# Kernel tuning notes

Hardware: AMD Instinct MI355X
Metric: run time of the kernel (lower is better)

Reference implementation:

```python
import jax, jax.numpy as jnp
import numpy as np

R = 4        # in_transformations == out_transformations
FS = 3       # filter_size
PAD = 1
STRIDE = 1


def setup_inputs() -> dict:
    key = jax.random.key(0)
    k1, k2, k3 = jax.random.split(key, 3)
    B, Cin, O, K = 16, 64, 64, 4
    Ctot = Cin * R  # 256
    x = jax.random.normal(k1, (B, Ctot, 64, 64), dtype=jnp.float32)
    # kernel bank: [num_dynamic_kernels, out_channels, in_channels, f, f]
    kernel_bank = jax.random.normal(k2, (K, O, Cin, FS, FS), dtype=jnp.float32) * 0.05
    # routing fc: Linear(total_in_channels -> num_kernels)
    fc_w = jax.random.normal(k3, (K, Ctot), dtype=jnp.float32) * 0.05
    fc_b = jnp.zeros((K,), dtype=jnp.float32)
    return {"x": x, "kernel_bank": kernel_bank, "fc_w": fc_w, "fc_b": fc_b}


def reference(x, kernel_bank, fc_w, fc_b):
    B, Ctot, H, W = x.shape
    K, O, Cin, f, _ = kernel_bank.shape
    # --- dynamic routing: global avg pool -> fc -> sigmoid ---
    pooled = x.mean(axis=(2, 3))                                  # [B, Ctot]
    coeffs = jax.nn.sigmoid(pooled @ fc_w.T + fc_b)               # [B, K]
    # --- per-sample kernel synthesis ---
    base = jnp.einsum('bk,kocij->bocij', coeffs, kernel_bank)     # [B, O, Cin, f, f]
    # rotations rot90^k for k in 0..R-1 (matches torch.rot90 dims=(-2,-1))
    rotated = jnp.stack([jnp.rot90(base, k, axes=(-2, -1)) for k in range(R)], axis=1)  # [B, R, O, Cin, f, f]
    # block kernel: block (r_out, r_in) uses rotation index (r_out - r_in) % R,
    # so the r_in sum of convs becomes one conv over all R*Cin input channels.
    r_out = jnp.arange(R)[:, None]
    r_in = jnp.arange(R)[None, :]
    idx = (r_out - r_in) % R                                      # [R, R]
    big = rotated[:, idx]                                         # [B, R_out, R_in, O, Cin, f, f]
    big = big.transpose(0, 1, 3, 2, 4, 5, 6).reshape(B, R * O, R * Cin, f, f)
    # --- per-sample conv (vmapped over batch; each sample has its own kernel) ---
    def conv_one(xi, wi):
        return jax.lax.conv_general_dilated(
            xi[None], wi,
            window_strides=(STRIDE, STRIDE),
            padding=[(PAD, PAD), (PAD, PAD)],
            dimension_numbers=('NCHW', 'OIHW', 'NCHW'))[0]
    return jax.vmap(conv_one)(x, big)                             # [B, R*O, H, W]
```

## Files before the change

kernel.cpp:

```cpp
#include <hip/hip_runtime.h>
#include <hip/hip_bf16.h>
#include <math.h>

#define BATCH 16
#define CT    256
#define HW    64
#define OCH   64
#define NK    4
#define HP    66
#define NPIX  4356

typedef __attribute__((ext_vector_type(4)))  float  f32x4;
typedef __attribute__((ext_vector_type(8)))  short  s16x8;
typedef __attribute__((ext_vector_type(4)))  unsigned short u16x4;

#define GLOBAL_AS __attribute__((address_space(1)))
#define LDS_AS    __attribute__((address_space(3)))

__device__ __constant__ int c_rotsrc[4][9] = {
    {0,1,2,3,4,5,6,7,8},
    {2,5,8,1,4,7,0,3,6},
    {8,7,6,5,4,3,2,1,0},
    {6,3,0,7,4,1,8,5,2}
};

static __device__ inline unsigned short f2bf(float f) {
    union { __hip_bfloat16 h; unsigned short u; } cv;
    cv.h = __float2bfloat16(f);
    return cv.u;
}

__global__ __launch_bounds__(256) void xpose_pool(const float* __restrict__ x,
                                                  unsigned short* __restrict__ xTg,
                                                  float* __restrict__ partial) {
    const int ci0 = blockIdx.x * 64;
    const int g0  = ci0 >> 3;
    const int pr  = blockIdx.y;
    const int b   = blockIdx.z;
    const int t   = threadIdx.x;

    if (pr == 0 || pr == HP-1) {
        for (int u = t; u < 8*HP; u += 256) {
            int g = u / HP, c = u % HP;
            *(s16x8*)(xTg + ((((size_t)(b*32 + g0 + g))*NPIX) + pr*HP + c)*8) =
                (s16x8)(short)0;
        }
        return;
    }
    const int r = pr - 1;

    __shared__ unsigned short tile[64][70];
    const int cilH = t >> 4;
    const int c0   = (t & 15) * 4;
    #pragma unroll
    for (int i = 0; i < 4; ++i) {
        int cil = cilH + i*16;
        f32x4 v = *(const f32x4*)(x + (((size_t)(b*CT + ci0 + cil))*HW + r)*HW + c0);
        tile[cil][c0+0] = f2bf(v[0]);
        tile[cil][c0+1] = f2bf(v[1]);
        tile[cil][c0+2] = f2bf(v[2]);
        tile[cil][c0+3] = f2bf(v[3]);
        float s = v[0] + v[1] + v[2] + v[3];
        s += __shfl_xor(s, 1, 16);
        s += __shfl_xor(s, 2, 16);
        s += __shfl_xor(s, 4, 16);
        s += __shfl_xor(s, 8, 16);
        if ((t & 15) == 0)
            partial[((size_t)(b*HW) + r)*CT + ci0 + cil] = s;
    }
    __syncthreads();

    if (t < 16) {
        int g = t & 7, side = t >> 3;
        *(s16x8*)(xTg + ((((size_t)(b*32 + g0 + g))*NPIX) + pr*HP + side*(HP-1))*8) =
            (s16x8)(short)0;
    }
    #pragma unroll
    for (int i = 0; i < 4; ++i) {
        int u = i*256 + t;
        int c = u & 63, cil0 = (u >> 6) * 4;
        u16x4 w;
        w[0] = tile[cil0+0][c];
        w[1] = tile[cil0+1][c];
        w[2] = tile[cil0+2][c];
        w[3] = tile[cil0+3][c];
        *(u16x4*)(xTg + ((((size_t)(b*32 + g0 + (cil0>>3)))*NPIX) + pr*HP + c + 1)*8
                  + (cil0 & 4)) = w;
    }
}

__global__ __launch_bounds__(256) void coeff_kernel(const float* __restrict__ partial,
                                                    const float* __restrict__ fc_w,
                                                    const float* __restrict__ fc_b,
                                                    float* __restrict__ coeffs) {
    const int b = blockIdx.x;
    const int t = threadIdx.x;
    const float* pp = partial + (size_t)b*HW*CT + t;
    float s = 0.f;
    #pragma unroll 8
    for (int r = 0; r < HW; ++r) s += pp[(size_t)r*CT];
    __shared__ float pool[CT];
    pool[t] = s * (1.f / (HW*HW));
    __syncthreads();
    const int w = t >> 6, l = t & 63;
    float d = 0.f;
    for (int c = l; c < CT; c += 64) d += pool[c] * fc_w[w*CT + c];
    for (int off = 32; off; off >>= 1) d += __shfl_down(d, off, 64);
    if (l == 0)
        coeffs[b*NK + w] = 1.f / (1.f + expf(-(d + fc_b[w])));
}

__global__ __launch_bounds__(256) void bankrot_kernel(const float* __restrict__ bank,
                                                      float* __restrict__ P) {
    const int idx = blockIdx.x * 256 + threadIdx.x;
    const int o = idx & 63;
    const int c = (idx >> 6) & 63;
    const int k = idx >> 12;
    const float* bp = bank + ((size_t)((k*OCH + o)*64 + c))*9;
    float v[9];
    #pragma unroll
    for (int s = 0; s < 9; ++s) v[s] = bp[s];
    #pragma unroll
    for (int rr = 0; rr < 4; ++rr)
        #pragma unroll
        for (int s = 0; s < 9; ++s)
            P[(size_t)(((k*4 + rr)*9 + s))*4096 + c*64 + o] = v[c_rotsrc[rr][s]];
}

__global__ __launch_bounds__(256) void wbuild_kernel(const float* __restrict__ coeffs,
                                                     const float* __restrict__ P,
                                                     unsigned short* __restrict__ Wb) {
    const int cig = blockIdx.x;
    const int s   = blockIdx.y;
    const int co  = threadIdx.x;
    const int ro  = co >> 6;
    const int o   = co & 63;
    const int ri  = cig >> 3;
    const int rr  = (ro - ri) & 3;
    const int c8  = (cig & 7) * 8;

    float r[NK][8];
    #pragma unroll
    for (int k = 0; k < NK; ++k) {
        const float* pp = P + (size_t)(((k*4 + rr)*9 + s))*4096 + o;
        #pragma unroll
        for (int q = 0; q < 8; ++q)
            r[k][q] = pp[(c8 + q)*64];
    }
    #pragma unroll
    for (int b = 0; b < BATCH; ++b) {
        const float cf0 = coeffs[b*NK+0], cf1 = coeffs[b*NK+1];
        const float cf2 = coeffs[b*NK+2], cf3 = coeffs[b*NK+3];
        s16x8 w;
        #pragma unroll
        for (int q = 0; q < 8; ++q) {
            float v = cf0*r[0][q] + cf1*r[1][q] + cf2*r[2][q] + cf3*r[3][q];
            w[q] = (short)f2bf(v);
        }
        *(s16x8*)(Wb + ((((size_t)(b*9 + s)*32 + cig)*256 + co) << 3)) = w;
    }
}

#define SLAB_U  266
#define CHUNK_U 1064
#define BUF_U   1088
#define MF(A_, B_, C_) __builtin_amdgcn_mfma_f32_16x16x32_bf16(A_, B_, C_, 0, 0, 0)

__global__ __launch_bounds__(128, 2) void conv_mfma(
        const unsigned short* __restrict__ xTg,
        const unsigned short* __restrict__ Wb,
        float* __restrict__ out) {
    const int bid  = blockIdx.x;
    const int b    = (bid & 7)*2 + ((bid >> 3) & 1);
    const int rest = bid >> 4;
    const int coT  = rest & 1;
    const int r0   = (rest >> 1) * 2;

    const int t    = threadIdx.x;
    const int w    = t >> 6;
    const int lane = t & 63;
    const int lo16 = lane & 15;
    const int hi4  = lane >> 4;

    __shared__ __align__(16) unsigned short Xs[2*BUF_U*8];

    f32x4 acc[4][8];
    #pragma unroll
    for (int f = 0; f < 4; ++f)
        #pragma unroll
        for (int p = 0; p < 8; ++p)
            acc[f][p] = (f32x4)0.f;

    const unsigned short* Wlane = Wb +
        (((size_t)(b*9*32) + hi4)*256 + coT*128 + w*64 + lo16)*8;

#define LOADA(DST, CH, S)                                                       \
    do {                                                                        \
        const unsigned short* wp = Wlane + (size_t)((S)*32 + (CH)*4)*2048;      \
        _Pragma("unroll")                                                       \
        for (int f_ = 0; f_ < 4; ++f_)                                          \
            DST[f_] = *(const s16x8*)(wp + f_*128);                             \
    } while (0)

#define STAGE(CH, BUF)                                                          \
    do {                                                                        \
        _Pragma("unroll")                                                       \
        for (int it = 0; it < 9; ++it) {                                        \
            int ubase = it*128 + w*64;                                          \
            if (ubase < CHUNK_U) {                                              \
                int u  = ubase + lane;                                          \
                int us = u > (CHUNK_U-3) ? (CHUNK_U-3) : u;  \
                int q  = us / SLAB_U;                                           \
                int pl = us - q*SLAB_U;                                         \
                const unsigned short* src = xTg +                               \
                    (((size_t)(b*32 + (CH)*4 + q))*NPIX + r0*HP + pl)*8;        \
                __builtin_amdgcn_global_load_lds(                               \
                    (const GLOBAL_AS void*)src,                                 \
                    (LDS_AS void*)(Xs + (size_t)((BUF)*BUF_U + ubase)*8),       \
                    16, 0, 0);                                                  \
            }                                                                   \
        }                                                                       \
    } while (0)

    STAGE(0, 0);
    __syncthreads();

    for (int ch = 0; ch < 8; ++ch) {
        s16x8 A[9][4];
        LOADA(A[0], ch, 0);
        LOADA(A[1], ch, 1);
        __builtin_amdgcn_sched_barrier(0);
        if (ch < 7) STAGE(ch+1, (ch+1) & 1);

        const char* Xb = (const char*)Xs + (ch & 1)*(BUF_U*16)
                         + hi4*(SLAB_U*16) + lo16*16;

        #pragma unroll
        for (int s = 0; s < 9; ++s) {
            if (s < 7) LOADA(A[s+2], ch, s+2);
            const int dr = s/3, dc = s%3;
            #pragma unroll
            for (int p = 0; p < 8; ++p) {
                const int pixbase = ((p>>2) + dr)*HP + dc + (p&3)*16;
                s16x8 bf = *(const s16x8*)(Xb + pixbase*16);
                acc[0][p] = MF(A[s][0], bf, acc[0][p]);
                acc[1][p] = MF(A[s][1], bf, acc[1][p]);
                acc[2][p] = MF(A[s][2], bf, acc[2][p]);
                acc[3][p] = MF(A[s][3], bf, acc[3][p]);
            }
        }
        __syncthreads();
    }
#undef STAGE
#undef LOADA

    #pragma unroll
    for (int f = 0; f < 4; ++f)
        #pragma unroll
        for (int p = 0; p < 8; ++p) {
            const int row  = r0 + (p >> 2);
            const int colb = (p & 3)*16 + lo16;
            #pragma unroll
            for (int j = 0; j < 4; ++j) {
                int co = coT*128 + w*64 + f*16 + hi4*4 + j;
                out[(((size_t)(b*CT + co))*HW + row)*HW + colb] = acc[f][p][j];
            }
        }
}

extern "C" void kernel_launch(void* const* d_in, const int* in_sizes, int n_in,
                              void* d_out, int out_size, void* d_ws, size_t ws_size,
                              hipStream_t stream) {
    const float* x    = (const float*)d_in[0];
    const float* bank = (const float*)d_in[1];
    const float* fc_w = (const float*)d_in[2];
    const float* fc_b = (const float*)d_in[3];
    float* out = (float*)d_out;

    char* wsb = (char*)d_ws;
    float* partial = (float*)wsb;
    float* Prot    = (float*)wsb;
    float* coeffs  = (float*)(wsb + 2359296);
    unsigned short* Wb  = (unsigned short*)(wsb + 2360320);
    unsigned short* xTg = (unsigned short*)(wsb + 21234688);

    xpose_pool<<<dim3(4, HP, BATCH), 256, 0, stream>>>(x, xTg, partial);
    coeff_kernel<<<BATCH, 256, 0, stream>>>(partial, fc_w, fc_b, coeffs);
    bankrot_kernel<<<64, 256, 0, stream>>>(bank, Prot);
    wbuild_kernel<<<dim3(32, 9), 256, 0, stream>>>(coeffs, Prot, Wb);
    conv_mfma<<<1024, 128, 0, stream>>>(xTg, Wb, out);
}
```

Baseline: 95.92 us.

## Interleave 32-channel groups per pixel in transposed input layout

Changes the bf16 transposed input layout from 8-channel slabs per pixel to 32 channels contiguous per pixel, so each conv chunk is one contiguous region in global memory. Staging into LDS becomes a simple linear copy, with no per-lane division or slab index math. The LDS read addressing is updated to match. It also prefetches one more weight stage ahead (three instead of two), which raises register pressure. Spreading 64-byte pixel strides across 16 lanes could cause LDS bank conflicts on the B-operand reads.

```diff
diff --git a/kernel.cpp b/kernel.cpp
--- a/kernel.cpp
+++ b/kernel.cpp
@@ -34,15 +34,17 @@
                                                   unsigned short* __restrict__ xTg,
                                                   float* __restrict__ partial) {
     const int ci0 = blockIdx.x * 64;
-    const int g0  = ci0 >> 3;
+    const int ch0 = ci0 >> 5;
     const int pr  = blockIdx.y;
     const int b   = blockIdx.z;
     const int t   = threadIdx.x;
 
     if (pr == 0 || pr == HP-1) {
-        for (int u = t; u < 8*HP; u += 256) {
-            int g = u / HP, c = u % HP;
-            *(s16x8*)(xTg + ((((size_t)(b*32 + g0 + g))*NPIX) + pr*HP + c)*8) =
+        for (int u = t; u < 528; u += 256) {
+            int chl = (u >= 264) ? 1 : 0;
+            int rem = u - chl*264;
+            int c = rem >> 2, q = rem & 3;
+            *(s16x8*)(xTg + (((size_t)(b*8 + ch0 + chl))*NPIX + pr*HP + c)*32 + q*8) =
                 (s16x8)(short)0;
         }
         return;
@@ -71,21 +73,22 @@
     __syncthreads();
 
     if (t < 16) {
-        int g = t & 7, side = t >> 3;
-        *(s16x8*)(xTg + ((((size_t)(b*32 + g0 + g))*NPIX) + pr*HP + side*(HP-1))*8) =
+        int side = t >> 3, r8 = t & 7;
+        int chl = r8 >> 2, q = r8 & 3;
+        *(s16x8*)(xTg + (((size_t)(b*8 + ch0 + chl))*NPIX + pr*HP + side*(HP-1))*32 + q*8) =
             (s16x8)(short)0;
     }
     #pragma unroll
     for (int i = 0; i < 4; ++i) {
-        int u = i*256 + t;
-        int c = u & 63, cil0 = (u >> 6) * 4;
+        const int chl = i >> 1;
+        const int c   = (i & 1)*32 + (t >> 3);
+        const int q   = t & 7;
         u16x4 w;
-        w[0] = tile[cil0+0][c];
-        w[1] = tile[cil0+1][c];
-        w[2] = tile[cil0+2][c];
-        w[3] = tile[cil0+3][c];
-        *(u16x4*)(xTg + ((((size_t)(b*32 + g0 + (cil0>>3)))*NPIX) + pr*HP + c + 1)*8
-                  + (cil0 & 4)) = w;
+        w[0] = tile[chl*32 + q*4 + 0][c];
+        w[1] = tile[chl*32 + q*4 + 1][c];
+        w[2] = tile[chl*32 + q*4 + 2][c];
+        w[3] = tile[chl*32 + q*4 + 3][c];
+        *(u16x4*)(xTg + (((size_t)(b*8 + ch0 + chl))*NPIX + pr*HP + c + 1)*32 + q*4) = w;
     }
 }
 
@@ -161,8 +164,7 @@
     }
 }
 
-#define SLAB_U  266
-#define CHUNK_U 1064
+#define CHUNK_U 1056
 #define BUF_U   1088
 #define MF(A_, B_, C_) __builtin_amdgcn_mfma_f32_16x16x32_bf16(A_, B_, C_, 0, 0, 0)
 
@@ -204,18 +206,16 @@
 
 #define STAGE(CH, BUF)                                                          \
     do {                                                                        \
+        const unsigned short* srcb = xTg +                                      \
+            (((size_t)(b*8 + (CH)))*NPIX + r0*HP)*32;                           \
         _Pragma("unroll")                                                       \
         for (int it = 0; it < 9; ++it) {                                        \
             int ubase = it*128 + w*64;                                          \
             if (ubase < CHUNK_U) {                                              \
                 int u  = ubase + lane;                                          \
-                int us = u > (CHUNK_U-3) ? (CHUNK_U-3) : u;  \
-                int q  = us / SLAB_U;                                           \
-                int pl = us - q*SLAB_U;                                         \
-                const unsigned short* src = xTg +                               \
-                    (((size_t)(b*32 + (CH)*4 + q))*NPIX + r0*HP + pl)*8;        \
+                int us = u > (CHUNK_U-1) ? (CHUNK_U-1) : u;  \
                 __builtin_amdgcn_global_load_lds(                               \
-                    (const GLOBAL_AS void*)src,                                 \
+                    (const GLOBAL_AS void*)(srcb + (size_t)us*8),               \
                     (LDS_AS void*)(Xs + (size_t)((BUF)*BUF_U + ubase)*8),       \
                     16, 0, 0);                                                  \
             }                                                                   \
@@ -229,20 +229,21 @@
         s16x8 A[9][4];
         LOADA(A[0], ch, 0);
         LOADA(A[1], ch, 1);
+        LOADA(A[2], ch, 2);
         __builtin_amdgcn_sched_barrier(0);
         if (ch < 7) STAGE(ch+1, (ch+1) & 1);
 
         const char* Xb = (const char*)Xs + (ch & 1)*(BUF_U*16)
-                         + hi4*(SLAB_U*16) + lo16*16;
+                         + lo16*64 + hi4*16;
 
         #pragma unroll
         for (int s = 0; s < 9; ++s) {
-            if (s < 7) LOADA(A[s+2], ch, s+2);
+            if (s < 6) LOADA(A[s+3], ch, s+3);
             const int dr = s/3, dc = s%3;
             #pragma unroll
             for (int p = 0; p < 8; ++p) {
-                const int pixbase = ((p>>2) + dr)*HP + dc + (p&3)*16;
-                s16x8 bf = *(const s16x8*)(Xb + pixbase*16);
+                const int pix = ((p>>2) + dr)*HP + dc + (p&3)*16;
+                s16x8 bf = *(const s16x8*)(Xb + pix*64);
                 acc[0][p] = MF(A[s][0], bf, acc[0][p]);
                 acc[1][p] = MF(A[s][1], bf, acc[1][p]);
                 acc[2][p] = MF(A[s][2], bf, acc[2][p]);
```

Measured after the change: 95.64 us. Within noise of the previous version (-0.3%).
